# Kernel optimization log

Hardware: AMD Instinct MI355X
Metric: run time of the kernel (lower is better)

The kernel has to match this reference:

```python
import jax, jax.numpy as jnp
import numpy as np

D_MODEL = 1024
N_STATE = 64
BASEWIDTH = 3
BC_SCALE = (D_MODEL / BASEWIDTH) ** -0.5  # 'mup' mode width_mult**-0.5
RMS_EPS = 1.1920928955078125e-07  # torch.finfo(float32).eps (RMSNorm eps=None default)


def setup_inputs() -> dict:
    key = jax.random.key(0)
    k1, k2, k3, k4 = jax.random.split(key, 4)
    Bsz, L = 4, 2048
    u = jax.random.normal(k1, (Bsz, D_MODEL, L), dtype=jnp.float32)
    A = jax.random.uniform(k2, (N_STATE,), dtype=jnp.float32) * 0.1  # buffer: rand(N)*A_scale
    B = (jax.random.normal(k3, (N_STATE, D_MODEL), dtype=jnp.float32) + 0.1) * BC_SCALE
    C = (jax.random.normal(k4, (N_STATE, D_MODEL), dtype=jnp.float32) + 0.1) * BC_SCALE
    D = jnp.ones((D_MODEL,), dtype=jnp.float32)
    norm_w = jnp.ones((D_MODEL,), dtype=jnp.float32)
    return {"L": L, "u": u, "A": A, "B": B, "C": C, "D": D, "norm_w": norm_w}


def _ssm(u, A, B, C, D, norm_w):
    # u: [b, d, l]
    scale = BC_SCALE  # applied to Bu, Cu in 'mup' hyperparam mode
    Bu = jnp.einsum('nd,bdl->bnl', B, u) * scale  # [b, n, l]
    Cu = jnp.einsum('nd,bdl->bnl', C, u) * scale  # [b, n, l]
    b, d, l = u.shape
    # shifted_delta == 1 (delta path commented out in source), so
    # h_{t} = A * h_{t-1} + Bu[:, :, t] (outer) u[:, :, t]
    h0 = jnp.zeros((b, d, A.shape[0]), dtype=u.dtype)

    def step(h, xs):
        bu_t, cu_t, u_t = xs  # [b,n], [b,n], [b,d]
        h = h * A + u_t[:, :, None] * bu_t[:, None, :]  # [b, d, n]
        y_t = jnp.einsum('bn,bdn->bd', cu_t, h)
        return h, y_t

    xs = (jnp.moveaxis(Bu, 2, 0), jnp.moveaxis(Cu, 2, 0), jnp.moveaxis(u, 2, 0))
    _, y = jax.lax.scan(step, h0, xs)  # y: [l, b, d]
    y = jnp.moveaxis(y, 0, 2).transpose(1, 0, 2) if False else jnp.transpose(y, (1, 2, 0))  # [b, d, l]
    out = y + u * D[None, :, None]
    # RMSNorm over d_model (apply in [b, l, d] layout)
    x = jnp.transpose(out, (0, 2, 1))  # [b, l, d]
    ms = jnp.mean(x * x, axis=-1, keepdims=True)
    x = x * jax.lax.rsqrt(ms + RMS_EPS) * norm_w
    return jnp.transpose(x, (0, 2, 1))  # [b, d, l]


def reference(L, u, A, B, C, D, norm_w):
    del L  # sequence length == u.shape[-1]
    return _ssm(u, A, B, C, D, norm_w)
```

## Files before the change

kernel.cpp:

```cpp
#include <hip/hip_runtime.h>
#include <stdint.h>

#define DM 1024
#define LS 2048
#define RMS_EPS 1.1920928955078125e-07f
#define S2 0.0029296875f

typedef __attribute__((ext_vector_type(8))) short bf16x8;
typedef __attribute__((ext_vector_type(4))) float f32x4;

__device__ __forceinline__ unsigned short f2bf(float f) {
  uint32_t u = __builtin_bit_cast(uint32_t, f);
  u += 0x7FFFu + ((u >> 16) & 1u);
  return (unsigned short)(u >> 16);
}

__global__ __launch_bounds__(256) void k0_prep(const float* __restrict__ B,
                                               const float* __restrict__ C,
                                               unsigned short* __restrict__ Bbf) {
  int i4 = blockIdx.x * 256 + threadIdx.x;
  const float4* src = (i4 < 16384) ? (const float4*)B : (const float4*)C;
  float4 v = src[i4 & 16383];
  ushort4 o;
  o.x = f2bf(v.x); o.y = f2bf(v.y); o.z = f2bf(v.z); o.w = f2bf(v.w);
  ((ushort4*)Bbf)[i4] = o;
}

__global__ __launch_bounds__(256) void k1_gemm(const float* __restrict__ u,
                                               const unsigned short* __restrict__ Bbf,
                                               float* __restrict__ BuCuT) {
  const int b    = blockIdx.y;
  const int l0   = blockIdx.x * 16;
  const int lane = threadIdx.x & 63;
  const int w    = threadIdx.x >> 6;
  const float* ub = u + (size_t)b * DM * LS;

  __shared__ bf16x8 tile[128][16];

  {
    const int lq = lane & 3;
    const int kg = lane >> 2;
    const int kbase = 256 * w + 16 * kg;
    #pragma unroll
    for (int h = 0; h < 2; ++h) {
      float4 vv[8];
      #pragma unroll
      for (int r = 0; r < 8; ++r)
        vv[r] = *(const float4*)(ub + (size_t)(kbase + 8*h + r) * LS + l0 + 4*lq);
      const int k8 = 32*w + 2*kg + h;
      #pragma unroll
      for (int c = 0; c < 4; ++c) {
        union { bf16x8 v; unsigned short s[8]; } t;
        #pragma unroll
        for (int r = 0; r < 8; ++r) t.s[r] = f2bf(((const float*)&vv[r])[c]);
        tile[k8][(4*lq + c) ^ (k8 & 3)] = t.v;
      }
    }
  }
  __syncthreads();

  const int n = lane & 15;
  const int q = lane >> 4;
  f32x4 acc[2] = {};
  #pragma unroll 4
  for (int it = 0; it < 32; ++it) {
    bf16x8 bfrag = tile[4*it + q][n ^ q];
    #pragma unroll
    for (int rt = 0; rt < 2; ++rt) {
      int row = 32*w + 16*rt + n;
      bf16x8 a = *(const bf16x8*)(Bbf + (size_t)row * DM + 32*it + 8*q);
      acc[rt] = __builtin_amdgcn_mfma_f32_16x16x32_bf16(a, bfrag, acc[rt], 0, 0, 0);
    }
  }

  float* ob = BuCuT + (size_t)b * LS * 128;
  #pragma unroll
  for (int rt = 0; rt < 2; ++rt) {
    int col = l0 + n;
    int row = 32*w + 16*rt + 4*q;
    *(f32x4*)(ob + (size_t)col * 128 + row) = acc[rt];
  }
}

__global__ __launch_bounds__(256) void k2_kw(const float* __restrict__ BuCuT,
                                             const float* __restrict__ A,
                                             float* __restrict__ Kw) {
  const int b  = blockIdx.y;
  const int t0 = blockIdx.x * 64;
  const int tl = threadIdx.x >> 2;
  const int p  = threadIdx.x & 3;
  const int t  = t0 + tl;
  const float* base = BuCuT + (size_t)b * LS * 128;

  float pw[16], aa[16];
  #pragma unroll
  for (int i = 0; i < 4; ++i) {
    float4 c4 = *(const float4*)(base + (size_t)t * 128 + 64 + 16*p + 4*i);
    float4 a4 = *(const float4*)(A + 16*p + 4*i);
    pw[4*i+0] = c4.x * S2; aa[4*i+0] = a4.x;
    pw[4*i+1] = c4.y * S2; aa[4*i+1] = a4.y;
    pw[4*i+2] = c4.z * S2; aa[4*i+2] = a4.z;
    pw[4*i+3] = c4.w * S2; aa[4*i+3] = a4.w;
  }
  float part[16];
  #pragma unroll
  for (int j = 0; j < 16; ++j) {
    float s = 0.f;
    if (t - j >= 0) {
      const float* bu = base + (size_t)(t - j) * 128 + 16*p;
      #pragma unroll
      for (int i = 0; i < 16; i += 4) {
        float4 b4 = *(const float4*)(bu + i);
        s = fmaf(pw[i+0], b4.x, s); s = fmaf(pw[i+1], b4.y, s);
        s = fmaf(pw[i+2], b4.z, s); s = fmaf(pw[i+3], b4.w, s);
      }
    }
    part[j] = s;
    #pragma unroll
    for (int i = 0; i < 16; ++i) pw[i] *= aa[i];
  }
  __shared__ float ss[64][68];
  #pragma unroll
  for (int j = 0; j < 16; ++j) ss[tl][p*17 + j] = part[j];
  __syncthreads();
  const int o  = threadIdx.x * 4;
  const int t2 = o >> 4;
  const int j0 = o & 15;
  float4 r;
  r.x = ss[t2][j0+0] + ss[t2][17+j0+0] + ss[t2][34+j0+0] + ss[t2][51+j0+0];
  r.y = ss[t2][j0+1] + ss[t2][17+j0+1] + ss[t2][34+j0+1] + ss[t2][51+j0+1];
  r.z = ss[t2][j0+2] + ss[t2][17+j0+2] + ss[t2][34+j0+2] + ss[t2][51+j0+2];
  r.w = ss[t2][j0+3] + ss[t2][17+j0+3] + ss[t2][34+j0+3] + ss[t2][51+j0+3];
  *(float4*)(Kw + ((size_t)b * LS + t0 + t2) * 16 + j0) = r;
}

__global__ __launch_bounds__(256) void k3_conv(const float* __restrict__ u,
                                               const float* __restrict__ Kw,
                                               const float* __restrict__ Dv,
                                               const float* __restrict__ nw,
                                               float* __restrict__ out) {
  const int b  = blockIdx.y;
  const int t0 = blockIdx.x * 16;
  const int tg = threadIdx.x & 3;
  const int dr = threadIdx.x >> 2;
  const float* ub = u + (size_t)b * DM * LS;
  float* ob = out + (size_t)b * DM * LS;

  float kw[4][16];
  #pragma unroll
  for (int k = 0; k < 4; ++k) {
    const float* kp = Kw + ((size_t)b * LS + t0 + 4*tg + k) * 16;
    #pragma unroll
    for (int i = 0; i < 4; ++i) {
      float4 v = *(const float4*)(kp + 4*i);
      kw[k][4*i+0] = v.x; kw[k][4*i+1] = v.y; kw[k][4*i+2] = v.z; kw[k][4*i+3] = v.w;
    }
  }

  const int cbase = t0 - 16 + 4*tg;
  float y[16][4];
  float ps[4] = {0.f, 0.f, 0.f, 0.f};
  #pragma unroll
  for (int c = 0; c < 16; ++c) {
    const int d = dr + 64*c;
    const float* row = ub + (size_t)d * LS;
    float wr[20];
    #pragma unroll
    for (int s5 = 0; s5 < 5; ++s5) {
      int g = cbase + 4*s5;
      float4 v;
      if (g >= 0) v = *(const float4*)(row + g);
      else        v = make_float4(0.f, 0.f, 0.f, 0.f);
      wr[4*s5+0] = v.x; wr[4*s5+1] = v.y; wr[4*s5+2] = v.z; wr[4*s5+3] = v.w;
    }
    const float Dd = Dv[d];
    #pragma unroll
    for (int k = 0; k < 4; ++k) {
      float acc = wr[16+k] * Dd;
      #pragma unroll
      for (int j = 0; j < 16; ++j)
        acc = fmaf(kw[k][j], wr[16 + k - j], acc);
      y[c][k] = acc;
      ps[k] = fmaf(acc, acc, ps[k]);
    }
  }

  __shared__ float ss[16][68];
  #pragma unroll
  for (int k = 0; k < 4; ++k) ss[4*tg + k][dr] = ps[k];
  __syncthreads();
  __shared__ float rsq[16];
  if (threadIdx.x < 16) {
    float s = 0.f;
    #pragma unroll
    for (int i = 0; i < 16; ++i) {
      float4 v = *(const float4*)&ss[threadIdx.x][4*i];
      s += (v.x + v.y) + (v.z + v.w);
    }
    rsq[threadIdx.x] = rsqrtf(s * (1.f/1024.f) + RMS_EPS);
  }
  __syncthreads();
  float rq[4];
  #pragma unroll
  for (int k = 0; k < 4; ++k) rq[k] = rsq[4*tg + k];
  #pragma unroll
  for (int c = 0; c < 16; ++c) {
    const int d = dr + 64*c;
    const float wn = nw[d];
    float4 o;
    o.x = y[c][0] * rq[0] * wn;
    o.y = y[c][1] * rq[1] * wn;
    o.z = y[c][2] * rq[2] * wn;
    o.w = y[c][3] * rq[3] * wn;
    *(float4*)(ob + (size_t)d * LS + t0 + 4*tg) = o;
  }
}

extern "C" void kernel_launch(void* const* d_in, const int* in_sizes, int n_in,
                              void* d_out, int out_size, void* d_ws, size_t ws_size,
                              hipStream_t stream) {
  const float* u  = (const float*)d_in[1];
  const float* A  = (const float*)d_in[2];
  const float* B  = (const float*)d_in[3];
  const float* C  = (const float*)d_in[4];
  const float* Dv = (const float*)d_in[5];
  const float* nw = (const float*)d_in[6];
  float* out = (float*)d_out;

  float* BuCuT = (float*)d_ws;
  float* Kw    = (float*)((char*)d_ws + (4u << 20));
  unsigned short* Bbf = (unsigned short*)((char*)d_ws + (4u << 20) + (512u << 10));

  k0_prep<<<dim3(128),    dim3(256), 0, stream>>>(B, C, Bbf);
  k1_gemm<<<dim3(128, 4), dim3(256), 0, stream>>>(u, Bbf, BuCuT);
  k2_kw  <<<dim3(32, 4),  dim3(256), 0, stream>>>(BuCuT, A, Kw);
  k3_conv<<<dim3(128, 4), dim3(256), 0, stream>>>(u, Kw, Dv, nw, out);
}
```

Baseline: 155.5 us.

## Widen gemm blocks, tile Kw computation in LDS, pack Kw to bf16, halve conv tiles

k1_gemm now runs 512 threads per block, each wave computing a single 16-row MFMA tile. k2_kw is restructured to stage Bu/Cu rows and powers of A in shared memory, with one output per thread and more blocks. Kw is stored as packed bf16 pairs, which halves its footprint. k3_conv processes 8 timesteps per block with 2 thread groups, doubling the grid to improve occupancy. The bf16 Kw adds rounding error to the convolution weights.

```diff
diff --git a/kernel.cpp b/kernel.cpp
--- a/kernel.cpp
+++ b/kernel.cpp
@@ -26,7 +26,7 @@
   ((ushort4*)Bbf)[i4] = o;
 }
 
-__global__ __launch_bounds__(256) void k1_gemm(const float* __restrict__ u,
+__global__ __launch_bounds__(512) void k1_gemm(const float* __restrict__ u,
                                                const unsigned short* __restrict__ Bbf,
                                                float* __restrict__ BuCuT) {
   const int b    = blockIdx.y;
@@ -40,160 +40,147 @@
   {
     const int lq = lane & 3;
     const int kg = lane >> 2;
-    const int kbase = 256 * w + 16 * kg;
-    #pragma unroll
-    for (int h = 0; h < 2; ++h) {
-      float4 vv[8];
+    const int k8 = 16*w + kg;
+    float4 vv[8];
+    #pragma unroll
+    for (int r = 0; r < 8; ++r)
+      vv[r] = *(const float4*)(ub + (size_t)(8*k8 + r) * LS + l0 + 4*lq);
+    #pragma unroll
+    for (int c = 0; c < 4; ++c) {
+      union { bf16x8 v; unsigned short s[8]; } t;
       #pragma unroll
-      for (int r = 0; r < 8; ++r)
-        vv[r] = *(const float4*)(ub + (size_t)(kbase + 8*h + r) * LS + l0 + 4*lq);
-      const int k8 = 32*w + 2*kg + h;
-      #pragma unroll
-      for (int c = 0; c < 4; ++c) {
-        union { bf16x8 v; unsigned short s[8]; } t;
-        #pragma unroll
-        for (int r = 0; r < 8; ++r) t.s[r] = f2bf(((const float*)&vv[r])[c]);
-        tile[k8][(4*lq + c) ^ (k8 & 3)] = t.v;
-      }
+      for (int r = 0; r < 8; ++r) t.s[r] = f2bf(((const float*)&vv[r])[c]);
+      tile[k8][(4*lq + c) ^ (k8 & 3)] = t.v;
     }
   }
   __syncthreads();
 
   const int n = lane & 15;
   const int q = lane >> 4;
-  f32x4 acc[2] = {};
+  f32x4 acc = {};
+  const unsigned short* arow = Bbf + (size_t)(16*w + n) * DM + 8*q;
   #pragma unroll 4
   for (int it = 0; it < 32; ++it) {
     bf16x8 bfrag = tile[4*it + q][n ^ q];
-    #pragma unroll
-    for (int rt = 0; rt < 2; ++rt) {
-      int row = 32*w + 16*rt + n;
-      bf16x8 a = *(const bf16x8*)(Bbf + (size_t)row * DM + 32*it + 8*q);
-      acc[rt] = __builtin_amdgcn_mfma_f32_16x16x32_bf16(a, bfrag, acc[rt], 0, 0, 0);
-    }
-  }
-
+    bf16x8 a = *(const bf16x8*)(arow + 32*it);
+    acc = __builtin_amdgcn_mfma_f32_16x16x32_bf16(a, bfrag, acc, 0, 0, 0);
+  }
   float* ob = BuCuT + (size_t)b * LS * 128;
-  #pragma unroll
-  for (int rt = 0; rt < 2; ++rt) {
-    int col = l0 + n;
-    int row = 32*w + 16*rt + 4*q;
-    *(f32x4*)(ob + (size_t)col * 128 + row) = acc[rt];
-  }
+  *(f32x4*)(ob + (size_t)(l0 + n) * 128 + 16*w + 4*q) = acc;
 }
 
 __global__ __launch_bounds__(256) void k2_kw(const float* __restrict__ BuCuT,
                                              const float* __restrict__ A,
-                                             float* __restrict__ Kw) {
-  const int b  = blockIdx.y;
-  const int t0 = blockIdx.x * 64;
-  const int tl = threadIdx.x >> 2;
-  const int p  = threadIdx.x & 3;
-  const int t  = t0 + tl;
-  const float* base = BuCuT + (size_t)b * LS * 128;
-
-  float pw[16], aa[16];
-  #pragma unroll
-  for (int i = 0; i < 4; ++i) {
-    float4 c4 = *(const float4*)(base + (size_t)t * 128 + 64 + 16*p + 4*i);
-    float4 a4 = *(const float4*)(A + 16*p + 4*i);
-    pw[4*i+0] = c4.x * S2; aa[4*i+0] = a4.x;
-    pw[4*i+1] = c4.y * S2; aa[4*i+1] = a4.y;
-    pw[4*i+2] = c4.z * S2; aa[4*i+2] = a4.z;
-    pw[4*i+3] = c4.w * S2; aa[4*i+3] = a4.w;
-  }
-  float part[16];
-  #pragma unroll
-  for (int j = 0; j < 16; ++j) {
-    float s = 0.f;
-    if (t - j >= 0) {
-      const float* bu = base + (size_t)(t - j) * 128 + 16*p;
-      #pragma unroll
-      for (int i = 0; i < 16; i += 4) {
-        float4 b4 = *(const float4*)(bu + i);
-        s = fmaf(pw[i+0], b4.x, s); s = fmaf(pw[i+1], b4.y, s);
-        s = fmaf(pw[i+2], b4.z, s); s = fmaf(pw[i+3], b4.w, s);
-      }
-    }
-    part[j] = s;
-    #pragma unroll
-    for (int i = 0; i < 16; ++i) pw[i] *= aa[i];
-  }
-  __shared__ float ss[64][68];
-  #pragma unroll
-  for (int j = 0; j < 16; ++j) ss[tl][p*17 + j] = part[j];
-  __syncthreads();
-  const int o  = threadIdx.x * 4;
-  const int t2 = o >> 4;
-  const int j0 = o & 15;
-  float4 r;
-  r.x = ss[t2][j0+0] + ss[t2][17+j0+0] + ss[t2][34+j0+0] + ss[t2][51+j0+0];
-  r.y = ss[t2][j0+1] + ss[t2][17+j0+1] + ss[t2][34+j0+1] + ss[t2][51+j0+1];
-  r.z = ss[t2][j0+2] + ss[t2][17+j0+2] + ss[t2][34+j0+2] + ss[t2][51+j0+2];
-  r.w = ss[t2][j0+3] + ss[t2][17+j0+3] + ss[t2][34+j0+3] + ss[t2][51+j0+3];
-  *(float4*)(Kw + ((size_t)b * LS + t0 + t2) * 16 + j0) = r;
-}
-
-__global__ __launch_bounds__(256) void k3_conv(const float* __restrict__ u,
-                                               const float* __restrict__ Kw,
-                                               const float* __restrict__ Dv,
-                                               const float* __restrict__ nw,
-                                               float* __restrict__ out) {
+                                             uint32_t* __restrict__ Kwp) {
   const int b  = blockIdx.y;
   const int t0 = blockIdx.x * 16;
-  const int tg = threadIdx.x & 3;
-  const int dr = threadIdx.x >> 2;
+  const int tid = threadIdx.x;
+  __shared__ float BuT[64][33];
+  __shared__ float CuT[64][33];
+  __shared__ float apow[64][17];
+  __shared__ float ss2[16][17];
+  const float* base = BuCuT + (size_t)b * LS * 128;
+
+  #pragma unroll
+  for (int i = 0; i < 4; ++i) {
+    int idx = tid + 256*i;
+    int rl  = idx >> 5;
+    int f4  = idx & 31;
+    int grow = t0 - 16 + rl;
+    float4 v = (grow >= 0) ? *(const float4*)(base + (size_t)grow * 128 + 4*f4)
+                           : make_float4(0.f, 0.f, 0.f, 0.f);
+    int c0 = 4*f4;
+    #pragma unroll
+    for (int e = 0; e < 4; ++e) {
+      int c = c0 + e;
+      float val = ((const float*)&v)[e];
+      if (c < 64) BuT[c][rl] = val; else CuT[c - 64][rl] = val;
+    }
+  }
+  if (tid < 64) {
+    float a = A[tid], p = 1.f;
+    #pragma unroll
+    for (int j = 0; j < 16; ++j) { apow[tid][j] = p; p *= a; }
+  }
+  __syncthreads();
+
+  const int t = tid & 15, j = tid >> 4;
+  const int rb = 16 + t - j;
+  float s = 0.f;
+  #pragma unroll 8
+  for (int n = 0; n < 64; ++n)
+    s = fmaf(CuT[n][16 + t] * apow[n][j], BuT[n][rb], s);
+  ss2[t][j] = s * S2;
+  __syncthreads();
+
+  if (tid < 128) {
+    int tt = tid >> 3, jp = tid & 7;
+    uint32_t pk = (uint32_t)f2bf(ss2[tt][2*jp])
+                | ((uint32_t)f2bf(ss2[tt][2*jp + 1]) << 16);
+    Kwp[((size_t)b * LS + t0 + tt) * 8 + jp] = pk;
+  }
+}
+
+__global__ __launch_bounds__(256, 4) void k3_conv(const float* __restrict__ u,
+                                                  const uint32_t* __restrict__ Kwp,
+                                                  const float* __restrict__ Dv,
+                                                  const float* __restrict__ nw,
+                                                  float* __restrict__ out) {
+  const int b  = blockIdx.y;
+  const int t0 = blockIdx.x * 8;
+  const int tg = threadIdx.x & 1;
+  const int dr = threadIdx.x >> 1;
   const float* ub = u + (size_t)b * DM * LS;
   float* ob = out + (size_t)b * DM * LS;
 
-  float kw[4][16];
+  uint32_t kwp[4][8];
   #pragma unroll
   for (int k = 0; k < 4; ++k) {
-    const float* kp = Kw + ((size_t)b * LS + t0 + 4*tg + k) * 16;
-    #pragma unroll
-    for (int i = 0; i < 4; ++i) {
-      float4 v = *(const float4*)(kp + 4*i);
-      kw[k][4*i+0] = v.x; kw[k][4*i+1] = v.y; kw[k][4*i+2] = v.z; kw[k][4*i+3] = v.w;
-    }
+    const uint32_t* kp = Kwp + ((size_t)b * LS + t0 + 4*tg + k) * 8;
+    *(uint4*)&kwp[k][0] = *(const uint4*)kp;
+    *(uint4*)&kwp[k][4] = *(const uint4*)(kp + 4);
   }
 
   const int cbase = t0 - 16 + 4*tg;
-  float y[16][4];
+  float y[8][4];
   float ps[4] = {0.f, 0.f, 0.f, 0.f};
   #pragma unroll
-  for (int c = 0; c < 16; ++c) {
-    const int d = dr + 64*c;
+  for (int c = 0; c < 8; ++c) {
+    const int d = dr + 128*c;
     const float* row = ub + (size_t)d * LS;
     float wr[20];
     #pragma unroll
     for (int s5 = 0; s5 < 5; ++s5) {
       int g = cbase + 4*s5;
-      float4 v;
-      if (g >= 0) v = *(const float4*)(row + g);
-      else        v = make_float4(0.f, 0.f, 0.f, 0.f);
+      float4 v = (g >= 0) ? *(const float4*)(row + g)
+                          : make_float4(0.f, 0.f, 0.f, 0.f);
       wr[4*s5+0] = v.x; wr[4*s5+1] = v.y; wr[4*s5+2] = v.z; wr[4*s5+3] = v.w;
     }
     const float Dd = Dv[d];
     #pragma unroll
     for (int k = 0; k < 4; ++k) {
-      float acc = wr[16+k] * Dd;
+      float acc = wr[16 + k] * Dd;
       #pragma unroll
-      for (int j = 0; j < 16; ++j)
-        acc = fmaf(kw[k][j], wr[16 + k - j], acc);
+      for (int jp = 0; jp < 8; ++jp) {
+        float klo = __builtin_bit_cast(float, kwp[k][jp] << 16);
+        float khi = __builtin_bit_cast(float, kwp[k][jp] & 0xffff0000u);
+        acc = fmaf(klo, wr[16 + k - 2*jp], acc);
+        acc = fmaf(khi, wr[16 + k - 2*jp - 1], acc);
+      }
       y[c][k] = acc;
       ps[k] = fmaf(acc, acc, ps[k]);
     }
   }
 
-  __shared__ float ss[16][68];
+  __shared__ float ss[8][132];
   #pragma unroll
   for (int k = 0; k < 4; ++k) ss[4*tg + k][dr] = ps[k];
   __syncthreads();
-  __shared__ float rsq[16];
-  if (threadIdx.x < 16) {
+  __shared__ float rsq[8];
+  if (threadIdx.x < 8) {
     float s = 0.f;
     #pragma unroll
-    for (int i = 0; i < 16; ++i) {
+    for (int i = 0; i < 32; ++i) {
       float4 v = *(const float4*)&ss[threadIdx.x][4*i];
       s += (v.x + v.y) + (v.z + v.w);
     }
@@ -204,8 +191,8 @@
   #pragma unroll
   for (int k = 0; k < 4; ++k) rq[k] = rsq[4*tg + k];
   #pragma unroll
-  for (int c = 0; c < 16; ++c) {
-    const int d = dr + 64*c;
+  for (int c = 0; c < 8; ++c) {
+    const int d = dr + 128*c;
     const float wn = nw[d];
     float4 o;
     o.x = y[c][0] * rq[0] * wn;
@@ -227,12 +214,12 @@
   const float* nw = (const float*)d_in[6];
   float* out = (float*)d_out;
 
-  float* BuCuT = (float*)d_ws;
-  float* Kw    = (float*)((char*)d_ws + (4u << 20));
-  unsigned short* Bbf = (unsigned short*)((char*)d_ws + (4u << 20) + (512u << 10));
+  float*    BuCuT = (float*)d_ws;
+  uint32_t* Kwp   = (uint32_t*)((char*)d_ws + (4u << 20));
+  unsigned short* Bbf = (unsigned short*)((char*)d_ws + (4u << 20) + (256u << 10));
 
   k0_prep<<<dim3(128),    dim3(256), 0, stream>>>(B, C, Bbf);
-  k1_gemm<<<dim3(128, 4), dim3(256), 0, stream>>>(u, Bbf, BuCuT);
-  k2_kw  <<<dim3(32, 4),  dim3(256), 0, stream>>>(BuCuT, A, Kw);
-  k3_conv<<<dim3(128, 4), dim3(256), 0, stream>>>(u, Kw, Dv, nw, out);
-}
+  k1_gemm<<<dim3(128, 4), dim3(512), 0, stream>>>(u, Bbf, BuCuT);
+  k2_kw  <<<dim3(128, 4), dim3(256), 0, stream>>>(BuCuT, A, Kwp);
+  k3_conv<<<dim3(256, 4), dim3(256), 0, stream>>>(u, Kwp, Dv, nw, out);
+}
```

Result: slower. 321.6 us (+106.8%).
